# Kernel tuning notes

Hardware: AMD Instinct MI355X
Metric: run time of the kernel (lower is better)

## Reference

```python
import jax, jax.numpy as jnp
import numpy as np

EPS = 1e-5


def _grid_sample_bilinear(feats, grid):
    """PyTorch F.grid_sample, mode='bilinear', padding_mode='zeros', align_corners=False.
    feats: (BN, C, H, W); grid: (BN, Q, 2) with (x, y) in [-1, 1]. Returns (BN, C, Q)."""
    BN, C, H, W = feats.shape
    # unnormalize (align_corners=False): pix = ((g + 1) * size - 1) / 2
    x = ((grid[..., 0] + 1.0) * W - 1.0) * 0.5
    y = ((grid[..., 1] + 1.0) * H - 1.0) * 0.5
    x0f = jnp.floor(x)
    y0f = jnp.floor(y)
    wx = x - x0f  # fractional weights
    wy = y - y0f
    x0 = x0f.astype(jnp.int32)
    y0 = y0f.astype(jnp.int32)
    feats_flat = feats.reshape(BN, C, H * W)

    def corner(ix, iy, w):
        valid = (ix >= 0) & (ix < W) & (iy >= 0) & (iy < H)
        lin = jnp.clip(iy, 0, H - 1) * W + jnp.clip(ix, 0, W - 1)  # (BN, Q)
        g = jnp.take_along_axis(feats_flat, lin[:, None, :], axis=2)  # (BN, C, Q)
        return g * (w * valid)[:, None, :]

    return (corner(x0, y0, (1.0 - wx) * (1.0 - wy))
            + corner(x0 + 1, y0, wx * (1.0 - wy))
            + corner(x0, y0 + 1, (1.0 - wx) * wy)
            + corner(x0 + 1, y0 + 1, wx * wy))


def reference(query, reference_points, image_features, lidar2img, W_out, b_out):
    B, Q, _ = reference_points.shape
    N = lidar2img.shape[1]
    _, _, C, H, W = image_features.shape

    # --- project_3d_to_2d ---
    pts = jnp.broadcast_to(reference_points[:, None], (B, N, Q, 3))
    homo = jnp.concatenate([pts, jnp.ones_like(pts[..., :1])], axis=-1)  # (B,N,Q,4)
    p2h = jnp.einsum('bnij,bnqj->bnqi', lidar2img, homo)  # (B,N,Q,4)
    z = p2h[..., 2:3]
    points_2d = p2h[..., 0:2] / (jnp.abs(z) + EPS)
    front_mask = (z > EPS)[..., 0]  # (B,N,Q)

    # --- feature_sampling ---
    gx = points_2d[..., 0] / (W - 1) * 2.0 - 1.0
    gy = points_2d[..., 1] / (H - 1) * 2.0 - 1.0
    grid = jnp.stack([gx, gy], axis=-1)  # (B,N,Q,2)
    sampled = _grid_sample_bilinear(
        image_features.reshape(B * N, C, H, W), grid.reshape(B * N, Q, 2))  # (BN,C,Q)
    sampled = sampled.reshape(B, N, C, Q).transpose(0, 3, 1, 2)  # (B,Q,N,C)

    in_image = jnp.maximum(jnp.abs(gx), jnp.abs(gy)) <= 1.0  # (B,N,Q)
    valid = (front_mask & in_image).transpose(0, 2, 1)[..., None]  # (B,Q,N,1)
    sampled = sampled * valid

    # --- aggregate over cameras + output projection (dropout = identity in eval) ---
    agg = sampled.mean(axis=2)  # (B,Q,C)
    return agg @ W_out.T + b_out


def setup_inputs() -> dict:
    key = jax.random.key(0)
    ks = jax.random.split(key, 5)
    B, N, Q, C, H, W = 2, 6, 900, 256, 116, 200
    query = jax.random.normal(ks[0], (B, Q, C), jnp.float32)
    reference_points = jax.random.uniform(ks[1], (B, Q, 3), dtype=jnp.float32)
    image_features = jax.random.normal(ks[2], (B, N, C, H, W), jnp.float32)
    # scale rows so projections land around the image plane with mostly positive depth
    raw = jax.random.uniform(ks[3], (B, N, 4, 4), dtype=jnp.float32)
    row_scale = jnp.array([float(W), float(H), 2.0, 1.0], jnp.float32)[None, None, :, None]
    lidar2img = raw * row_scale
    W_out = jax.random.normal(ks[4], (C, C), jnp.float32) / np.sqrt(C).astype(np.float32)
    b_out = jnp.zeros((C,), jnp.float32)
    return {"query": query, "reference_points": reference_points,
            "image_features": image_features, "lidar2img": lidar2img,
            "W_out": W_out, "b_out": b_out}
```

## Files before the change

kernel.cpp:

```cpp
#include <hip/hip_runtime.h>
#include <hip/hip_bf16.h>
#include <cstdint>

#define Bb 2
#define Nc 6
#define Qn 900
#define Cc 256
#define Hc 116
#define Wc 200
#define EPSf 1e-5f

struct Proj { int x0, y0; float wx, wy; };

__global__ void proj_kernel(const float* __restrict__ ref_pts,
                            const float* __restrict__ l2i,
                            Proj* __restrict__ proj) {
    int t = blockIdx.x * blockDim.x + threadIdx.x;
    if (t >= Bb * Nc * Qn) return;
    int q  = t % Qn;
    int bn = t / Qn;
    int b  = bn / Nc;

    const float* p = ref_pts + ((size_t)b * Qn + q) * 3;
    float px = p[0], py = p[1], pz = p[2];
    const float* M = l2i + (size_t)bn * 16;
    float h0 = M[0]*px + M[1]*py + M[2]*pz  + M[3];
    float h1 = M[4]*px + M[5]*py + M[6]*pz  + M[7];
    float h2 = M[8]*px + M[9]*py + M[10]*pz + M[11];

    float denom = fabsf(h2) + EPSf;
    float x2d = h0 / denom;
    float y2d = h1 / denom;
    float gx = x2d / (float)(Wc - 1) * 2.0f - 1.0f;
    float gy = y2d / (float)(Hc - 1) * 2.0f - 1.0f;
    bool front = h2 > EPSf;
    bool in_img = fmaxf(fabsf(gx), fabsf(gy)) <= 1.0f;

    Proj o;
    if (front && in_img) {
        float x = ((gx + 1.0f) * (float)Wc - 1.0f) * 0.5f;
        float y = ((gy + 1.0f) * (float)Hc - 1.0f) * 0.5f;
        float x0f = floorf(x), y0f = floorf(y);
        o.x0 = (int)x0f;
        o.y0 = (int)y0f;
        o.wx = x - x0f;
        o.wy = y - y0f;
    } else {
        o.x0 = INT32_MIN; o.y0 = 0; o.wx = 0.0f; o.wy = 0.0f;
    }
    proj[t] = o;
}

__global__ void sample_kernel(const float* __restrict__ feats,
                              const Proj* __restrict__ proj,
                              float* __restrict__ agg) {
    int bq = blockIdx.x;
    int b  = bq / Qn;
    int q  = bq % Qn;
    int c  = threadIdx.x;

    float acc = 0.0f;
    #pragma unroll
    for (int n = 0; n < Nc; ++n) {
        int bn = b * Nc + n;
        Proj pr = proj[(size_t)bn * Qn + q];
        if (pr.x0 == INT32_MIN) continue;

        const float* img = feats + ((size_t)bn * Cc + c) * (size_t)(Hc * Wc);
        int x0 = pr.x0, y0 = pr.y0, x1 = x0 + 1, y1 = y0 + 1;
        float wx = pr.wx, wy = pr.wy;

        bool vx0 = (x0 >= 0) & (x0 < Wc);
        bool vx1 = (x1 >= 0) & (x1 < Wc);
        bool vy0 = (y0 >= 0) & (y0 < Hc);
        bool vy1 = (y1 >= 0) & (y1 < Hc);
        int cx0 = min(max(x0, 0), Wc - 1);
        int cx1 = min(max(x1, 0), Wc - 1);
        int cy0 = min(max(y0, 0), Hc - 1);
        int cy1 = min(max(y1, 0), Hc - 1);

        float v00 = img[cy0 * Wc + cx0] * ((vx0 & vy0) ? 1.0f : 0.0f);
        float v01 = img[cy0 * Wc + cx1] * ((vx1 & vy0) ? 1.0f : 0.0f);
        float v10 = img[cy1 * Wc + cx0] * ((vx0 & vy1) ? 1.0f : 0.0f);
        float v11 = img[cy1 * Wc + cx1] * ((vx1 & vy1) ? 1.0f : 0.0f);

        acc += (v00 * (1.0f - wx) + v01 * wx) * (1.0f - wy)
             + (v10 * (1.0f - wx) + v11 * wx) * wy;
    }
    agg[(size_t)bq * Cc + c] = acc * (1.0f / 6.0f);
}

#define QT 8
__global__ void out_gemm(const float* __restrict__ agg,
                         const float* __restrict__ Wm,
                         const float* __restrict__ bias,
                         float* __restrict__ out) {
    __shared__ float sA[QT][Cc];
    int base_q = blockIdx.x * QT;
    int tid = threadIdx.x;

    for (int i = tid; i < QT * Cc; i += 256)
        sA[i / Cc][i % Cc] = agg[(size_t)base_q * Cc + i];
    __syncthreads();

    float acc[QT];
    #pragma unroll
    for (int j = 0; j < QT; ++j) acc[j] = 0.0f;

    const float4* wrow = (const float4*)(Wm + (size_t)tid * Cc);
    #pragma unroll 4
    for (int c4 = 0; c4 < Cc / 4; ++c4) {
        float4 w = wrow[c4];
        #pragma unroll
        for (int j = 0; j < QT; ++j) {
            acc[j] += w.x * sA[j][4*c4 + 0] + w.y * sA[j][4*c4 + 1]
                    + w.z * sA[j][4*c4 + 2] + w.w * sA[j][4*c4 + 3];
        }
    }
    float bb = bias[tid];
    #pragma unroll
    for (int j = 0; j < QT; ++j)
        out[(size_t)(base_q + j) * Cc + tid] = acc[j] + bb;
}

extern "C" void kernel_launch(void* const* d_in, const int* in_sizes, int n_in,
                              void* d_out, int out_size, void* d_ws, size_t ws_size,
                              hipStream_t stream) {
    const float* ref_pts = (const float*)d_in[1];
    const float* feats   = (const float*)d_in[2];
    const float* l2i     = (const float*)d_in[3];
    const float* Wm      = (const float*)d_in[4];
    const float* bias    = (const float*)d_in[5];
    float* out = (float*)d_out;

    size_t proj_bytes = (size_t)Bb * Nc * Qn * sizeof(Proj);
    proj_bytes = (proj_bytes + 255) & ~(size_t)255;
    Proj*  proj = (Proj*)d_ws;
    float* agg  = (float*)((char*)d_ws + proj_bytes);

    int npts = Bb * Nc * Qn;
    proj_kernel<<<(npts + 255) / 256, 256, 0, stream>>>(ref_pts, l2i, proj);
    sample_kernel<<<Bb * Qn, 256, 0, stream>>>(feats, proj, agg);
    out_gemm<<<(Bb * Qn) / QT, 256, 0, stream>>>(agg, Wm, bias, out);
}
```

Measured before the change: 399.8 us.

## Transpose image features to channel-last before bilinear sampling

Result: slower. 457.3 us (+14.4%).

```diff
diff --git a/kernel.cpp b/kernel.cpp
--- a/kernel.cpp
+++ b/kernel.cpp
@@ -8,6 +8,7 @@
 #define Cc 256
 #define Hc 116
 #define Wc 200
+#define Pp (Hc * Wc)
 #define EPSf 1e-5f
 
 struct Proj { int x0, y0; float wx, wy; };
@@ -51,6 +52,83 @@
     proj[t] = o;
 }
 
+__global__ void transpose_kernel(const float* __restrict__ in,
+                                 float* __restrict__ out) {
+    __shared__ float s[64][65];
+    int bn = blockIdx.z;
+    int c0 = blockIdx.y * 64;
+    int p0 = blockIdx.x * 64;
+    int tid = threadIdx.x;
+
+    int lp = (tid & 15) * 4;
+    int lc = tid >> 4;
+    const float* src = in + ((size_t)bn * Cc + c0) * Pp + p0;
+    bool full = (p0 + 64 <= Pp);
+
+    #pragma unroll
+    for (int i = 0; i < 4; ++i) {
+        int c = lc + i * 16;
+        if (full || (lp < Pp - p0)) {
+            float4 v = *(const float4*)(src + (size_t)c * Pp + lp);
+            s[c][lp + 0] = v.x; s[c][lp + 1] = v.y;
+            s[c][lp + 2] = v.z; s[c][lp + 3] = v.w;
+        }
+    }
+    __syncthreads();
+
+    int wc = (tid & 15) * 4;
+    int wp = tid >> 4;
+    float* dst = out + ((size_t)bn * Pp + p0) * Cc + c0;
+    #pragma unroll
+    for (int i = 0; i < 4; ++i) {
+        int p = wp + i * 16;
+        if (full || (p < Pp - p0)) {
+            float4 v = make_float4(s[wc + 0][p], s[wc + 1][p],
+                                   s[wc + 2][p], s[wc + 3][p]);
+            *(float4*)(dst + (size_t)p * Cc + wc) = v;
+        }
+    }
+}
+
+__global__ void sample_kernel_t(const float* __restrict__ featsT,
+                                const Proj* __restrict__ proj,
+                                float* __restrict__ agg) {
+    int bq = blockIdx.x;
+    int b  = bq / Qn;
+    int q  = bq % Qn;
+    int c  = threadIdx.x;
+
+    float acc = 0.0f;
+    #pragma unroll
+    for (int n = 0; n < Nc; ++n) {
+        int bn = b * Nc + n;
+        Proj pr = proj[(size_t)bn * Qn + q];
+        if (pr.x0 == INT32_MIN) continue;
+
+        int x0 = pr.x0, y0 = pr.y0, x1 = x0 + 1, y1 = y0 + 1;
+        float wx = pr.wx, wy = pr.wy;
+
+        bool vx0 = (x0 >= 0) & (x0 < Wc);
+        bool vx1 = (x1 >= 0) & (x1 < Wc);
+        bool vy0 = (y0 >= 0) & (y0 < Hc);
+        bool vy1 = (y1 >= 0) & (y1 < Hc);
+        int cx0 = min(max(x0, 0), Wc - 1);
+        int cx1 = min(max(x1, 0), Wc - 1);
+        int cy0 = min(max(y0, 0), Hc - 1);
+        int cy1 = min(max(y1, 0), Hc - 1);
+
+        const float* base = featsT + (size_t)bn * Pp * Cc + c;
+        float v00 = base[(size_t)(cy0 * Wc + cx0) * Cc] * ((vx0 & vy0) ? 1.0f : 0.0f);
+        float v01 = base[(size_t)(cy0 * Wc + cx1) * Cc] * ((vx1 & vy0) ? 1.0f : 0.0f);
+        float v10 = base[(size_t)(cy1 * Wc + cx0) * Cc] * ((vx0 & vy1) ? 1.0f : 0.0f);
+        float v11 = base[(size_t)(cy1 * Wc + cx1) * Cc] * ((vx1 & vy1) ? 1.0f : 0.0f);
+
+        acc += (v00 * (1.0f - wx) + v01 * wx) * (1.0f - wy)
+             + (v10 * (1.0f - wx) + v11 * wx) * wy;
+    }
+    agg[(size_t)bq * Cc + c] = acc * (1.0f / 6.0f);
+}
+
 __global__ void sample_kernel(const float* __restrict__ feats,
                               const Proj* __restrict__ proj,
                               float* __restrict__ agg) {
@@ -66,7 +144,7 @@
         Proj pr = proj[(size_t)bn * Qn + q];
         if (pr.x0 == INT32_MIN) continue;
 
-        const float* img = feats + ((size_t)bn * Cc + c) * (size_t)(Hc * Wc);
+        const float* img = feats + ((size_t)bn * Cc + c) * (size_t)Pp;
         int x0 = pr.x0, y0 = pr.y0, x1 = x0 + 1, y1 = y0 + 1;
         float wx = pr.wx, wy = pr.wy;
 
@@ -135,11 +213,24 @@
 
     size_t proj_bytes = (size_t)Bb * Nc * Qn * sizeof(Proj);
     proj_bytes = (proj_bytes + 255) & ~(size_t)255;
+    size_t agg_bytes = (size_t)Bb * Qn * Cc * sizeof(float);
+    agg_bytes = (agg_bytes + 255) & ~(size_t)255;
+    size_t featsT_bytes = (size_t)Bb * Nc * Pp * Cc * sizeof(float);
+
     Proj*  proj = (Proj*)d_ws;
     float* agg  = (float*)((char*)d_ws + proj_bytes);
 
     int npts = Bb * Nc * Qn;
     proj_kernel<<<(npts + 255) / 256, 256, 0, stream>>>(ref_pts, l2i, proj);
-    sample_kernel<<<Bb * Qn, 256, 0, stream>>>(feats, proj, agg);
+
+    if (ws_size >= proj_bytes + agg_bytes + featsT_bytes) {
+        float* featsT = (float*)((char*)d_ws + proj_bytes + agg_bytes);
+        dim3 tgrid((Pp + 63) / 64, Cc / 64, Bb * Nc);
+        transpose_kernel<<<tgrid, 256, 0, stream>>>(feats, featsT);
+        sample_kernel_t<<<Bb * Qn, 256, 0, stream>>>(featsT, proj, agg);
+    } else {
+        sample_kernel<<<Bb * Qn, 256, 0, stream>>>(feats, proj, agg);
+    }
+
     out_gemm<<<(Bb * Qn) / QT, 256, 0, stream>>>(agg, Wm, bias, out);
 }
```

## Split camera loop into per-camera sample blocks and reduce cameras in GEMM

Applied to the files above, without the earlier changes.

Result: faster. 379.6 us (-5.1%).

```diff
diff --git a/kernel.cpp b/kernel.cpp
--- a/kernel.cpp
+++ b/kernel.cpp
@@ -1,5 +1,4 @@
 #include <hip/hip_runtime.h>
-#include <hip/hip_bf16.h>
 #include <cstdint>
 
 #define Bb 2
@@ -8,6 +7,7 @@
 #define Cc 256
 #define Hc 116
 #define Wc 200
+#define Pp (Hc * Wc)
 #define EPSf 1e-5f
 
 struct Proj { int x0, y0; float wx, wy; };
@@ -51,47 +51,44 @@
     proj[t] = o;
 }
 
-__global__ void sample_kernel(const float* __restrict__ feats,
-                              const Proj* __restrict__ proj,
-                              float* __restrict__ agg) {
-    int bq = blockIdx.x;
-    int b  = bq / Qn;
-    int q  = bq % Qn;
-    int c  = threadIdx.x;
+__global__ void sample1_kernel(const float* __restrict__ feats,
+                               const Proj* __restrict__ proj,
+                               float* __restrict__ samp) {
+    int blk = blockIdx.x;
+    int c   = threadIdx.x;
+    size_t ob = (size_t)blk * Cc + c;
 
-    float acc = 0.0f;
-    #pragma unroll
-    for (int n = 0; n < Nc; ++n) {
-        int bn = b * Nc + n;
-        Proj pr = proj[(size_t)bn * Qn + q];
-        if (pr.x0 == INT32_MIN) continue;
+    Proj pr = proj[blk];
+    if (pr.x0 == INT32_MIN) {
+        samp[ob] = 0.0f;
+        return;
+    }
+    int bn = blk / Qn;
 
-        const float* img = feats + ((size_t)bn * Cc + c) * (size_t)(Hc * Wc);
-        int x0 = pr.x0, y0 = pr.y0, x1 = x0 + 1, y1 = y0 + 1;
-        float wx = pr.wx, wy = pr.wy;
+    const float* img = feats + ((size_t)bn * Cc + c) * (size_t)Pp;
+    int x0 = pr.x0, y0 = pr.y0, x1 = x0 + 1, y1 = y0 + 1;
+    float wx = pr.wx, wy = pr.wy;
 
-        bool vx0 = (x0 >= 0) & (x0 < Wc);
-        bool vx1 = (x1 >= 0) & (x1 < Wc);
-        bool vy0 = (y0 >= 0) & (y0 < Hc);
-        bool vy1 = (y1 >= 0) & (y1 < Hc);
-        int cx0 = min(max(x0, 0), Wc - 1);
-        int cx1 = min(max(x1, 0), Wc - 1);
-        int cy0 = min(max(y0, 0), Hc - 1);
-        int cy1 = min(max(y1, 0), Hc - 1);
+    bool vx0 = (x0 >= 0) & (x0 < Wc);
+    bool vx1 = (x1 >= 0) & (x1 < Wc);
+    bool vy0 = (y0 >= 0) & (y0 < Hc);
+    bool vy1 = (y1 >= 0) & (y1 < Hc);
+    int cx0 = min(max(x0, 0), Wc - 1);
+    int cx1 = min(max(x1, 0), Wc - 1);
+    int cy0 = min(max(y0, 0), Hc - 1);
+    int cy1 = min(max(y1, 0), Hc - 1);
 
-        float v00 = img[cy0 * Wc + cx0] * ((vx0 & vy0) ? 1.0f : 0.0f);
-        float v01 = img[cy0 * Wc + cx1] * ((vx1 & vy0) ? 1.0f : 0.0f);
-        float v10 = img[cy1 * Wc + cx0] * ((vx0 & vy1) ? 1.0f : 0.0f);
-        float v11 = img[cy1 * Wc + cx1] * ((vx1 & vy1) ? 1.0f : 0.0f);
+    float v00 = img[cy0 * Wc + cx0] * ((vx0 & vy0) ? 1.0f : 0.0f);
+    float v01 = img[cy0 * Wc + cx1] * ((vx1 & vy0) ? 1.0f : 0.0f);
+    float v10 = img[cy1 * Wc + cx0] * ((vx0 & vy1) ? 1.0f : 0.0f);
+    float v11 = img[cy1 * Wc + cx1] * ((vx1 & vy1) ? 1.0f : 0.0f);
 
-        acc += (v00 * (1.0f - wx) + v01 * wx) * (1.0f - wy)
+    samp[ob] = (v00 * (1.0f - wx) + v01 * wx) * (1.0f - wy)
              + (v10 * (1.0f - wx) + v11 * wx) * wy;
-    }
-    agg[(size_t)bq * Cc + c] = acc * (1.0f / 6.0f);
 }
 
 #define QT 8
-__global__ void out_gemm(const float* __restrict__ agg,
+__global__ void out_gemm(const float* __restrict__ samp,
                          const float* __restrict__ Wm,
                          const float* __restrict__ bias,
                          float* __restrict__ out) {
@@ -99,8 +96,19 @@
     int base_q = blockIdx.x * QT;
     int tid = threadIdx.x;
 
-    for (int i = tid; i < QT * Cc; i += 256)
-        sA[i / Cc][i % Cc] = agg[(size_t)base_q * Cc + i];
+    for (int i = tid; i < QT * Cc; i += 256) {
+        int j = i >> 8;
+        int c = i & 255;
+        int row = base_q + j;
+        int b  = row / Qn;
+        int qq = row - b * Qn;
+        const float* sp = samp + ((size_t)(b * Nc) * Qn + qq) * Cc + c;
+        float s = 0.0f;
+        #pragma unroll
+        for (int n = 0; n < Nc; ++n)
+            s += sp[(size_t)n * Qn * Cc];
+        sA[j][c] = s * (1.0f / 6.0f);
+    }
     __syncthreads();
 
     float acc[QT];
@@ -135,11 +143,12 @@
 
     size_t proj_bytes = (size_t)Bb * Nc * Qn * sizeof(Proj);
     proj_bytes = (proj_bytes + 255) & ~(size_t)255;
+
     Proj*  proj = (Proj*)d_ws;
-    float* agg  = (float*)((char*)d_ws + proj_bytes);
+    float* samp = (float*)((char*)d_ws + proj_bytes);
 
     int npts = Bb * Nc * Qn;
     proj_kernel<<<(npts + 255) / 256, 256, 0, stream>>>(ref_pts, l2i, proj);
-    sample_kernel<<<Bb * Qn, 256, 0, stream>>>(feats, proj, agg);
-    out_gemm<<<(Bb * Qn) / QT, 256, 0, stream>>>(agg, Wm, bias, out);
+    sample1_kernel<<<npts, 256, 0, stream>>>(feats, proj, samp);
+    out_gemm<<<(Bb * Qn) / QT, 256, 0, stream>>>(samp, Wm, bias, out);
 }
```
